# Performance work log

Hardware: AMD Instinct MI355X
Metric: run time of the kernel (lower is better)

## Reference

```python
import jax, jax.numpy as jnp
import numpy as np

N_HEADS = 2
OUT_DIM = 128
HEAD_DIM = OUT_DIM // N_HEADS
LN_EPS = 1e-5


def setup_inputs() -> dict:
    key = jax.random.key(0)
    ks = jax.random.split(key, 12)
    B, N = 8192, 32
    node_dim, edge_dim, time_dim = 172, 172, 100
    s_q = (node_dim + time_dim) ** -0.5
    s_kv = (node_dim + edge_dim + time_dim) ** -0.5
    s_o = OUT_DIM ** -0.5
    return {
        "node_feat": jax.random.normal(ks[0], (B, node_dim), jnp.float32),
        "time_feat": jax.random.normal(ks[1], (B, time_dim), jnp.float32),
        "edge_feat": jax.random.normal(ks[2], (B, N, edge_dim), jnp.float32),
        "nbr_node_feat": jax.random.normal(ks[3], (B, N, node_dim), jnp.float32),
        "nbr_time_feat": jax.random.normal(ks[4], (B, N, time_dim), jnp.float32),
        "nbr_mask": jax.random.randint(ks[5], (B, N), 0, 2, jnp.int32),
        "Wq": jax.random.normal(ks[6], (OUT_DIM, node_dim + time_dim), jnp.float32) * s_q,
        "bq": jnp.zeros((OUT_DIM,), jnp.float32),
        "Wkv": jax.random.normal(ks[7], (2 * OUT_DIM, node_dim + edge_dim + time_dim), jnp.float32) * s_kv,
        "bkv": jnp.zeros((2 * OUT_DIM,), jnp.float32),
        "Wo": jax.random.normal(ks[8], (OUT_DIM, OUT_DIM), jnp.float32) * s_o,
        "bo": jnp.zeros((OUT_DIM,), jnp.float32),
        "gamma": jnp.ones((OUT_DIM,), jnp.float32),
        "beta": jnp.zeros((OUT_DIM,), jnp.float32),
    }


def reference(node_feat, time_feat, edge_feat, nbr_node_feat, nbr_time_feat,
              nbr_mask, Wq, bq, Wkv, bkv, Wo, bo, gamma, beta):
    B = node_feat.shape[0]
    # Q projection: [B, out_dim]
    Q = jnp.concatenate([node_feat, time_feat], axis=-1) @ Wq.T + bq
    # KV projection: [B, N, 2*out_dim]
    Z = jnp.concatenate([nbr_node_feat, edge_feat, nbr_time_feat], axis=-1) @ Wkv.T + bkv
    # NOTE: faithful to torch: plain reshape of [B, N, out_dim] -> [B, H, N, d]
    # (mixes neighbor/head axes; identical row-major semantics in jnp)
    K = Z[:, :, :OUT_DIM].reshape(B, N_HEADS, -1, HEAD_DIM)
    V = Z[:, :, OUT_DIM:].reshape(B, N_HEADS, -1, HEAD_DIM)
    Qh = Q.reshape(B, N_HEADS, 1, HEAD_DIM)
    A = jnp.einsum('bhld,bhnd->bhln', Qh, K) * (HEAD_DIM ** -0.5)  # [B,H,1,N]
    pad = (nbr_mask == 0).reshape(B, 1, 1, -1)
    A = jnp.where(pad, jnp.float32(-1e10), A)
    A = jax.nn.softmax(A, axis=-1)  # dropout is identity at inference
    O = jnp.einsum('bhln,bhnd->bhld', A, V).reshape(B, OUT_DIM)
    out = O @ Wo.T + bo
    mu = jnp.mean(out, axis=-1, keepdims=True)
    var = jnp.mean(jnp.square(out - mu), axis=-1, keepdims=True)
    return (out - mu) * jax.lax.rsqrt(var + LN_EPS) * gamma + beta
```

## Files before the change

### kernel.cpp

```cpp
#include <hip/hip_runtime.h>
#include <hip/hip_bf16.h>

typedef __attribute__((ext_vector_type(4))) float f32x4;
typedef __attribute__((ext_vector_type(8))) short short8;
typedef __attribute__((ext_vector_type(8))) __bf16 bf16x8;

#define NDIM 172
#define EDIM 172
#define TDIM 100
#define KCAT 444
#define QDIM 272
#define ODIM 128
#define ZDIM 256
#define NNBR 32
#define NPH 14
#define NT 7
#define RPB 8
#define LN_EPS 1e-5f

#define Z_OFF    0
#define A_OFF    65536
#define QRES_OFF 73728
#define MASK_OFF 77824
#define PB_OFF   78848
#define OB_OFF   79872
#define RED_OFF  81920
#define SMEM_BYTES 81984

#define ZB(r,c) ((((r) * 512) + ((c) * 2)) ^ (((r) & 7) << 4))

#define BARRIER() do { \
    asm volatile("s_waitcnt lgkmcnt(0)\ns_barrier" ::: "memory"); \
    __builtin_amdgcn_sched_barrier(0); \
} while (0)

__device__ __forceinline__ unsigned short f2bf(float f) {
    unsigned u = __builtin_bit_cast(unsigned, f);
    u += 0x7fffu + ((u >> 16) & 1u);
    return (unsigned short)(u >> 16);
}
__device__ __forceinline__ float bf2f(unsigned short h) {
    unsigned u = ((unsigned)h) << 16;
    return __builtin_bit_cast(float, u);
}
__device__ __forceinline__ unsigned short bfb(float f) {
    return __builtin_bit_cast(unsigned short, (__bf16)f);
}

#define WFRAG_N (NPH * 8192)
#define WQT_N (QDIM * ODIM)
#define WOT_N (ODIM * ODIM)
__global__ void prep_pack(const float* __restrict__ Wkv, const float* __restrict__ Wq,
                          const float* __restrict__ Wo,
                          unsigned short* __restrict__ wfrag,
                          unsigned short* __restrict__ wqT,
                          unsigned short* __restrict__ woT) {
    int idx = blockIdx.x * 256 + threadIdx.x;
    if (idx < WFRAG_N) {
        int phase = idx >> 13;
        int r = idx & 8191;
        int n16 = r >> 9;
        int q = r & 511;
        int l = q >> 3, e = q & 7;
        int row = n16 * 16 + (l & 15);
        int k = phase * 32 + ((l >> 4) << 3) + e;
        wfrag[idx] = f2bf(k < KCAT ? Wkv[row * KCAT + k] : 0.f);
    } else if (idx < WFRAG_N + WQT_N) {
        int j = idx - WFRAG_N;
        int k = j >> 7, c = j & 127;
        wqT[j] = f2bf(Wq[c * QDIM + k]);
    } else if (idx < WFRAG_N + WQT_N + WOT_N) {
        int j = idx - WFRAG_N - WQT_N;
        int k = j >> 7, c = j & 127;
        woT[j] = f2bf(Wo[c * ODIM + k]);
    }
}

__global__ __launch_bounds__(256) void q_proj(
    const float* __restrict__ node_feat, const float* __restrict__ time_feat,
    const unsigned short* __restrict__ wqT, const float* __restrict__ bq,
    float* __restrict__ Qbuf) {
    __shared__ float x[8][QDIM];
    const int tid = threadIdx.x;
    const long b0 = (long)blockIdx.x * 8;
    for (int g = tid; g < 8 * QDIM; g += 256) {
        int r = g / QDIM, k = g - r * QDIM;
        x[r][k] = (k < NDIM) ? node_feat[(b0 + r) * NDIM + k]
                             : time_feat[(b0 + r) * TDIM + (k - NDIM)];
    }
    __syncthreads();
    const int c = tid & 127;
    const int rb = (tid >> 7) * 4;
    float s0 = bq[c], s1 = s0, s2 = s0, s3 = s0;
    #pragma unroll 8
    for (int k = 0; k < QDIM; k++) {
        float w = bf2f(wqT[k * 128 + c]);
        s0 += x[rb + 0][k] * w;
        s1 += x[rb + 1][k] * w;
        s2 += x[rb + 2][k] * w;
        s3 += x[rb + 3][k] * w;
    }
    Qbuf[(b0 + rb + 0) * 128 + c] = s0;
    Qbuf[(b0 + rb + 1) * 128 + c] = s1;
    Qbuf[(b0 + rb + 2) * 128 + c] = s2;
    Qbuf[(b0 + rb + 3) * 128 + c] = s3;
}

__global__ __launch_bounds__(512, 2) void ta_fused(
    const float* __restrict__ edge_feat, const float* __restrict__ nbr_node,
    const float* __restrict__ nbr_time, const int* __restrict__ nbr_mask,
    const float* __restrict__ Qbuf,
    const unsigned short* __restrict__ wfrag, const float* __restrict__ bkv,
    const unsigned short* __restrict__ woT, const float* __restrict__ bo,
    const float* __restrict__ gamma, const float* __restrict__ beta,
    float* __restrict__ out)
{
    extern __shared__ __align__(16) unsigned char smem[];
    float* qresL = (float*)(smem + QRES_OFF);
    int*   maskL = (int*)(smem + MASK_OFF);
    float* Pband = (float*)(smem + PB_OFF);
    float* Obuf  = (float*)(smem + OB_OFF);
    float* red   = (float*)(smem + RED_OFF);

    const int tid  = threadIdx.x;
    const int lane = tid & 63;
    const int wid  = tid >> 6;
    const int b0   = blockIdx.x * RPB;

    if (tid < RPB * NNBR) maskL[tid] = nbr_mask[(long)b0 * NNBR + tid];
    qresL[tid]       = Qbuf[(long)b0 * ODIM + tid];
    qresL[tid + 512] = Qbuf[(long)b0 * ODIM + tid + 512];
    __syncthreads();

    bf16x8 Wr[2 * NPH];
    #pragma unroll
    for (int p = 0; p < NPH; p++)
        #pragma unroll
        for (int j = 0; j < 2; j++)
            Wr[p * 2 + j] = __builtin_bit_cast(bf16x8,
                *(const short8*)(wfrag + ((size_t)(p * 16 + wid * 2 + j) * 512 + lane * 8)));
    const float bk0 = bkv[wid * 32 + (lane & 15)];
    const float bk1 = bkv[wid * 32 + 16 + (lane & 15)];

    const int rowA  = tid >> 4;
    const int kgrp4 = (tid & 15) * 4;
    const int awb   = ((rowA * 128 + (tid & 15) * 8) ^ ((rowA & 7) << 4));

    auto loadA = [&](int riX, int t) -> float4 {
        int k = t * 64 + kgrp4;
        long rg = ((long)b0 + riX) * NNBR + rowA;
        const float* p; int off;
        if (k < NDIM)             { p = nbr_node  + rg * NDIM; off = k; }
        else if (k < NDIM + EDIM) { p = edge_feat + rg * EDIM; off = k - NDIM; }
        else { p = nbr_time + rg * TDIM; off = k - NDIM - EDIM;
               if (off > TDIM - 4) off = TDIM - 4; }
        return *(const float4*)(p + off);
    };

    float4 rs[NT];
    #pragma unroll
    for (int t = 0; t < NT; t++) rs[t] = loadA(0, t);
    __builtin_amdgcn_sched_barrier(0);

    for (int ri = 0; ri < RPB; ri++) {
        const int riN = (ri + 1 < RPB) ? ri + 1 : RPB - 1;
        f32x4 acc[2][2];
        #pragma unroll
        for (int m = 0; m < 2; m++)
            #pragma unroll
            for (int n = 0; n < 2; n++) acc[m][n] = (f32x4){0.f, 0.f, 0.f, 0.f};

        #pragma unroll
        for (int t = 0; t < NT; t++) {
            unsigned char* aw = smem + A_OFF + (t & 1) * 4096;
            {
                float4 v = rs[t];
                uint2 w;
                w.x = (unsigned)bfb(v.x) | ((unsigned)bfb(v.y) << 16);
                w.y = (unsigned)bfb(v.z) | ((unsigned)bfb(v.w) << 16);
                *(uint2*)(aw + awb) = w;
            }
            rs[t] = loadA(riN, t);
            __builtin_amdgcn_sched_barrier(0);
            BARRIER();
            #pragma unroll
            for (int kk = 0; kk < 2; kk++) {
                bf16x8 af[2];
                #pragma unroll
                for (int m = 0; m < 2; m++) {
                    int row = m * 16 + (lane & 15);
                    af[m] = __builtin_bit_cast(bf16x8, *(const short8*)(
                        aw + row * 128 + ((kk * 64 + (lane >> 4) * 16) ^ ((row & 7) << 4))));
                }
                const int p = t * 2 + kk;
                acc[0][0] = __builtin_amdgcn_mfma_f32_16x16x32_bf16(af[0], Wr[p*2+0], acc[0][0], 0, 0, 0);
                acc[0][1] = __builtin_amdgcn_mfma_f32_16x16x32_bf16(af[0], Wr[p*2+1], acc[0][1], 0, 0, 0);
                acc[1][0] = __builtin_amdgcn_mfma_f32_16x16x32_bf16(af[1], Wr[p*2+0], acc[1][0], 0, 0, 0);
                acc[1][1] = __builtin_amdgcn_mfma_f32_16x16x32_bf16(af[1], Wr[p*2+1], acc[1][1], 0, 0, 0);
            }
        }

        const int gi = ri & 3;
        #pragma unroll
        for (int n = 0; n < 2; n++) {
            int col = wid * 32 + n * 16 + (lane & 15);
            float bk = n ? bk1 : bk0;
            #pragma unroll
            for (int m = 0; m < 2; m++)
                #pragma unroll
                for (int j = 0; j < 4; j++) {
                    int rowZ = gi * 32 + m * 16 + (lane >> 4) * 4 + j;
                    *(unsigned short*)(smem + ZB(rowZ, col)) = bfb(acc[m][n][j] + bk);
                }
        }

        if (gi == 3) {
            const int g = ri >> 2;
            BARRIER();

            {
                int bl = wid >> 1, h = wid & 1;
                int n2 = lane >> 1, half = lane & 1;
                int np = h * 16 + (n2 >> 1);
                int rowZ = bl * NNBR + np;
                int cb = (n2 & 1) * 64 + half * 32;
                const float* q = qresL + (g * 4 + bl) * ODIM + h * 64 + half * 32;
                float s = 0.f;
                #pragma unroll
                for (int j = 0; j < 4; j++) {
                    short8 z8 = *(const short8*)(smem + ZB(rowZ, cb + j * 8));
                    #pragma unroll
                    for (int e = 0; e < 8; e++)
                        s += q[j * 8 + e] * bf2f((unsigned short)z8[e]);
                }
                s += __shfl_xor(s, 1);
                s *= 0.125f;
                if (maskL[(g * 4 + bl) * NNBR + n2] == 0) s = -1e10f;
                float mx = s;
                #pragma unroll
                for (int off = 1; off < 64; off <<= 1) mx = fmaxf(mx, __shfl_xor(mx, off));
                float e = __expf(s - mx);
                float sum = e;
                #pragma unroll
                for (int off = 1; off < 64; off <<= 1) sum += __shfl_xor(sum, off);
                float pv = e * 2.f / sum;
                if (half == 0) Pband[(bl * 2 + h) * NNBR + n2] = pv;
            }
            BARRIER();

            {
                int b = tid >> 7, c = tid & 127, h = c >> 6, d = c & 63;
                const float* P = Pband + (b * 2 + h) * NNBR;
                float s = 0.f;
                #pragma unroll
                for (int n2 = 0; n2 < NNBR; n2++) {
                    int np = h * 16 + (n2 >> 1);
                    int col = ODIM + (n2 & 1) * 64 + d;
                    s += P[n2] * bf2f(*(const unsigned short*)(smem + ZB(b * NNBR + np, col)));
                }
                Obuf[b * ODIM + c] = s;
            }
            BARRIER();

            {
                int b = tid >> 7, c = tid & 127;
                float s = bo[c];
                const float* ob = Obuf + b * ODIM;
                #pragma unroll 8
                for (int k = 0; k < ODIM; k++)
                    s += ob[k] * bf2f(woT[k * 128 + c]);
                float s1 = s, s2 = s * s;
                #pragma unroll
                for (int off = 1; off < 64; off <<= 1) {
                    s1 += __shfl_xor(s1, off);
                    s2 += __shfl_xor(s2, off);
                }
                if (lane == 0) { red[wid * 2] = s1; red[wid * 2 + 1] = s2; }
                BARRIER();
                float t1 = red[b * 4 + 0] + red[b * 4 + 2];
                float t2 = red[b * 4 + 1] + red[b * 4 + 3];
                float mu  = t1 * (1.f / 128.f);
                float var = t2 * (1.f / 128.f) - mu * mu;
                float inv = rsqrtf(var + LN_EPS);
                out[(long)(b0 + g * 4 + b) * ODIM + c] = (s - mu) * inv * gamma[c] + beta[c];
            }
            BARRIER();
        }
    }
}

extern "C" void kernel_launch(void* const* d_in, const int* in_sizes, int n_in,
                              void* d_out, int out_size, void* d_ws, size_t ws_size,
                              hipStream_t stream) {
    const float* node_feat = (const float*)d_in[0];
    const float* time_feat = (const float*)d_in[1];
    const float* edge_feat = (const float*)d_in[2];
    const float* nbr_node  = (const float*)d_in[3];
    const float* nbr_time  = (const float*)d_in[4];
    const int*   nbr_mask  = (const int*)d_in[5];
    const float* Wq   = (const float*)d_in[6];
    const float* bq   = (const float*)d_in[7];
    const float* Wkv  = (const float*)d_in[8];
    const float* bkv  = (const float*)d_in[9];
    const float* Wo   = (const float*)d_in[10];
    const float* bo   = (const float*)d_in[11];
    const float* gma  = (const float*)d_in[12];
    const float* bta  = (const float*)d_in[13];
    float* out = (float*)d_out;

    const int B = in_sizes[0] / NDIM;

    char* ws = (char*)d_ws;
    float* Qbuf = (float*)ws;
    unsigned short* wfrag = (unsigned short*)(ws + (size_t)B * ODIM * 4);
    unsigned short* wqT   = wfrag + WFRAG_N;
    unsigned short* woT   = wqT + WQT_N;

    hipFuncSetAttribute((const void*)ta_fused,
                        hipFuncAttributeMaxDynamicSharedMemorySize, SMEM_BYTES);

    const int prep_total = WFRAG_N + WQT_N + WOT_N;
    prep_pack<<<dim3((prep_total + 255) / 256), dim3(256), 0, stream>>>(
        Wkv, Wq, Wo, wfrag, wqT, woT);
    q_proj<<<dim3(B / 8), dim3(256), 0, stream>>>(node_feat, time_feat, wqT, bq, Qbuf);
    ta_fused<<<dim3(B / RPB), dim3(512), SMEM_BYTES, stream>>>(
        edge_feat, nbr_node, nbr_time, nbr_mask, Qbuf,
        wfrag, bkv, woT, bo, gma, bta, out);
}
```

Measured before the change: 179.3 us.

## Double fused-kernel block to 1024 threads, halving per-wave KV output columns

```diff
diff --git a/kernel.cpp b/kernel.cpp
--- a/kernel.cpp
+++ b/kernel.cpp
@@ -25,7 +25,7 @@
 #define PB_OFF   78848
 #define OB_OFF   79872
 #define RED_OFF  81920
-#define SMEM_BYTES 81984
+#define SMEM_BYTES 82048
 
 #define ZB(r,c) ((((r) * 512) + ((c) * 2)) ^ (((r) & 7) << 4))
 
@@ -106,7 +106,7 @@
     Qbuf[(b0 + rb + 3) * 128 + c] = s3;
 }
 
-__global__ __launch_bounds__(512, 2) void ta_fused(
+__global__ __launch_bounds__(1024, 4) void ta_fused(
     const float* __restrict__ edge_feat, const float* __restrict__ nbr_node,
     const float* __restrict__ nbr_time, const int* __restrict__ nbr_mask,
     const float* __restrict__ Qbuf,
@@ -128,57 +128,50 @@
     const int b0   = blockIdx.x * RPB;
 
     if (tid < RPB * NNBR) maskL[tid] = nbr_mask[(long)b0 * NNBR + tid];
-    qresL[tid]       = Qbuf[(long)b0 * ODIM + tid];
-    qresL[tid + 512] = Qbuf[(long)b0 * ODIM + tid + 512];
+    qresL[tid] = Qbuf[(long)b0 * ODIM + tid];
     __syncthreads();
 
-    bf16x8 Wr[2 * NPH];
+    bf16x8 Wr[NPH];
     #pragma unroll
     for (int p = 0; p < NPH; p++)
-        #pragma unroll
-        for (int j = 0; j < 2; j++)
-            Wr[p * 2 + j] = __builtin_bit_cast(bf16x8,
-                *(const short8*)(wfrag + ((size_t)(p * 16 + wid * 2 + j) * 512 + lane * 8)));
-    const float bk0 = bkv[wid * 32 + (lane & 15)];
-    const float bk1 = bkv[wid * 32 + 16 + (lane & 15)];
-
-    const int rowA  = tid >> 4;
-    const int kgrp4 = (tid & 15) * 4;
-    const int awb   = ((rowA * 128 + (tid & 15) * 8) ^ ((rowA & 7) << 4));
-
-    auto loadA = [&](int riX, int t) -> float4 {
-        int k = t * 64 + kgrp4;
+        Wr[p] = __builtin_bit_cast(bf16x8,
+            *(const short8*)(wfrag + ((size_t)(p * 16 + wid) * 512 + lane * 8)));
+    const float bkW = bkv[wid * 16 + (lane & 15)];
+
+    const int rowA = tid >> 5;
+    const int kg   = tid & 31;
+    const int awb  = rowA * 128 + ((kg * 4) ^ ((rowA & 7) << 4));
+
+    auto loadA = [&](int riX, int t) -> float2 {
+        int k = t * 64 + kg * 2;
         long rg = ((long)b0 + riX) * NNBR + rowA;
         const float* p; int off;
         if (k < NDIM)             { p = nbr_node  + rg * NDIM; off = k; }
         else if (k < NDIM + EDIM) { p = edge_feat + rg * EDIM; off = k - NDIM; }
         else { p = nbr_time + rg * TDIM; off = k - NDIM - EDIM;
-               if (off > TDIM - 4) off = TDIM - 4; }
-        return *(const float4*)(p + off);
+               if (off > TDIM - 2) off = TDIM - 2; }
+        return *(const float2*)(p + off);
     };
 
-    float4 rs[NT];
+    float2 rs[NT];
     #pragma unroll
     for (int t = 0; t < NT; t++) rs[t] = loadA(0, t);
     __builtin_amdgcn_sched_barrier(0);
 
     for (int ri = 0; ri < RPB; ri++) {
         const int riN = (ri + 1 < RPB) ? ri + 1 : RPB - 1;
-        f32x4 acc[2][2];
-        #pragma unroll
-        for (int m = 0; m < 2; m++)
-            #pragma unroll
-            for (int n = 0; n < 2; n++) acc[m][n] = (f32x4){0.f, 0.f, 0.f, 0.f};
+        const int sp  = ri & 1;
+        f32x4 acc[2];
+        acc[0] = (f32x4){0.f, 0.f, 0.f, 0.f};
+        acc[1] = (f32x4){0.f, 0.f, 0.f, 0.f};
 
         #pragma unroll
         for (int t = 0; t < NT; t++) {
-            unsigned char* aw = smem + A_OFF + (t & 1) * 4096;
+            unsigned char* aw = smem + A_OFF + (((t + sp) & 1) ? 4096 : 0);
             {
-                float4 v = rs[t];
-                uint2 w;
-                w.x = (unsigned)bfb(v.x) | ((unsigned)bfb(v.y) << 16);
-                w.y = (unsigned)bfb(v.z) | ((unsigned)bfb(v.w) << 16);
-                *(uint2*)(aw + awb) = w;
+                float2 v = rs[t];
+                unsigned w = (unsigned)bfb(v.x) | ((unsigned)bfb(v.y) << 16);
+                *(unsigned*)(aw + awb) = w;
             }
             rs[t] = loadA(riN, t);
             __builtin_amdgcn_sched_barrier(0);
@@ -192,25 +185,20 @@
                     af[m] = __builtin_bit_cast(bf16x8, *(const short8*)(
                         aw + row * 128 + ((kk * 64 + (lane >> 4) * 16) ^ ((row & 7) << 4))));
                 }
-                const int p = t * 2 + kk;
-                acc[0][0] = __builtin_amdgcn_mfma_f32_16x16x32_bf16(af[0], Wr[p*2+0], acc[0][0], 0, 0, 0);
-                acc[0][1] = __builtin_amdgcn_mfma_f32_16x16x32_bf16(af[0], Wr[p*2+1], acc[0][1], 0, 0, 0);
-                acc[1][0] = __builtin_amdgcn_mfma_f32_16x16x32_bf16(af[1], Wr[p*2+0], acc[1][0], 0, 0, 0);
-                acc[1][1] = __builtin_amdgcn_mfma_f32_16x16x32_bf16(af[1], Wr[p*2+1], acc[1][1], 0, 0, 0);
+                acc[0] = __builtin_amdgcn_mfma_f32_16x16x32_bf16(af[0], Wr[t * 2 + kk], acc[0], 0, 0, 0);
+                acc[1] = __builtin_amdgcn_mfma_f32_16x16x32_bf16(af[1], Wr[t * 2 + kk], acc[1], 0, 0, 0);
             }
         }
 
         const int gi = ri & 3;
-        #pragma unroll
-        for (int n = 0; n < 2; n++) {
-            int col = wid * 32 + n * 16 + (lane & 15);
-            float bk = n ? bk1 : bk0;
+        {
+            int col = wid * 16 + (lane & 15);
             #pragma unroll
             for (int m = 0; m < 2; m++)
                 #pragma unroll
                 for (int j = 0; j < 4; j++) {
                     int rowZ = gi * 32 + m * 16 + (lane >> 4) * 4 + j;
-                    *(unsigned short*)(smem + ZB(rowZ, col)) = bfb(acc[m][n][j] + bk);
+                    *(unsigned short*)(smem + ZB(rowZ, col)) = bfb(acc[m][j] + bkW);
                 }
         }
 
@@ -218,7 +206,7 @@
             const int g = ri >> 2;
             BARRIER();
 
-            {
+            if (wid < 8) {
                 int bl = wid >> 1, h = wid & 1;
                 int n2 = lane >> 1, half = lane & 1;
                 int np = h * 16 + (n2 >> 1);
@@ -248,7 +236,7 @@
             }
             BARRIER();
 
-            {
+            if (tid < 512) {
                 int b = tid >> 7, c = tid & 127, h = c >> 6, d = c & 63;
                 const float* P = Pband + (b * 2 + h) * NNBR;
                 float s = 0.f;
@@ -263,26 +251,31 @@
             BARRIER();
 
             {
-                int b = tid >> 7, c = tid & 127;
-                float s = bo[c];
-                const float* ob = Obuf + b * ODIM;
-                #pragma unroll 8
-                for (int k = 0; k < ODIM; k++)
-                    s += ob[k] * bf2f(woT[k * 128 + c]);
+                int b = (tid >> 7) & 3, c = tid & 127;
+                float s = 0.f;
+                if (tid < 512) {
+                    s = bo[c];
+                    const float* ob = Obuf + b * ODIM;
+                    #pragma unroll 8
+                    for (int k = 0; k < ODIM; k++)
+                        s += ob[k] * bf2f(woT[k * 128 + c]);
+                }
                 float s1 = s, s2 = s * s;
                 #pragma unroll
                 for (int off = 1; off < 64; off <<= 1) {
                     s1 += __shfl_xor(s1, off);
                     s2 += __shfl_xor(s2, off);
                 }
-                if (lane == 0) { red[wid * 2] = s1; red[wid * 2 + 1] = s2; }
+                if (tid < 512 && lane == 0) { red[wid * 2] = s1; red[wid * 2 + 1] = s2; }
                 BARRIER();
-                float t1 = red[b * 4 + 0] + red[b * 4 + 2];
-                float t2 = red[b * 4 + 1] + red[b * 4 + 3];
-                float mu  = t1 * (1.f / 128.f);
-                float var = t2 * (1.f / 128.f) - mu * mu;
-                float inv = rsqrtf(var + LN_EPS);
-                out[(long)(b0 + g * 4 + b) * ODIM + c] = (s - mu) * inv * gamma[c] + beta[c];
+                if (tid < 512) {
+                    float t1 = red[b * 4 + 0] + red[b * 4 + 2];
+                    float t2 = red[b * 4 + 1] + red[b * 4 + 3];
+                    float mu  = t1 * (1.f / 128.f);
+                    float var = t2 * (1.f / 128.f) - mu * mu;
+                    float inv = rsqrtf(var + LN_EPS);
+                    out[(long)(b0 + g * 4 + b) * ODIM + c] = (s - mu) * inv * gamma[c] + beta[c];
+                }
             }
             BARRIER();
         }
@@ -323,7 +316,7 @@
     prep_pack<<<dim3((prep_total + 255) / 256), dim3(256), 0, stream>>>(
         Wkv, Wq, Wo, wfrag, wqT, woT);
     q_proj<<<dim3(B / 8), dim3(256), 0, stream>>>(node_feat, time_feat, wqT, bq, Qbuf);
-    ta_fused<<<dim3(B / RPB), dim3(512), SMEM_BYTES, stream>>>(
+    ta_fused<<<dim3(B / RPB), dim3(1024), SMEM_BYTES, stream>>>(
         edge_feat, nbr_node, nbr_time, nbr_mask, Qbuf,
         wfrag, bkv, woT, bo, gma, bta, out);
 }
```

After: 503.1 us. +180.6%, slower.
